# Kernel optimization log

Measured on AMD Instinct MI355X. Metric: run time of the kernel, lower is better.

## Reference

```python
import jax, jax.numpy as jnp
import numpy as np

DT = 0.001  # fixed dt in SimplifiedSSM.forward
LN_EPS = 1e-5


def _layernorm(x, g, b):
    m = jnp.mean(x, axis=-1, keepdims=True)
    v = jnp.mean(jnp.square(x - m), axis=-1, keepdims=True)
    return (x - m) * jax.lax.rsqrt(v + LN_EPS) * g + b


def setup_inputs() -> dict:
    key = jax.random.key(0)
    ks = jax.random.split(key, 12)
    Bn, C, H, W = 8, 1024, 32, 32
    depth, S = 4, 128
    d = C
    inp = {
        "x": jax.random.normal(ks[0], (Bn, C, H, W), dtype=jnp.float32),
        # SSM params, stacked over depth. A scaled by 0.1 for numerical stability
        # of the length-1024 recurrence (same math, tamer eigenvalues).
        "A": 0.1 * jax.random.normal(ks[1], (depth, S, S), dtype=jnp.float32),
        "Bp": jax.random.normal(ks[2], (depth, S, d), dtype=jnp.float32),
        "Cp": jax.random.normal(ks[3], (depth, d, S), dtype=jnp.float32),
        "Dp": jax.random.normal(ks[4], (depth, d), dtype=jnp.float32),
        # Linear layers (PyTorch convention: y = x @ W.T + b)
        "Wi": jax.random.normal(ks[5], (depth, d, d), dtype=jnp.float32) / np.sqrt(d),
        "bi": jax.random.normal(ks[6], (depth, d), dtype=jnp.float32) * 0.01,
        "Wo": jax.random.normal(ks[7], (depth, d, d), dtype=jnp.float32) / np.sqrt(d),
        "bo": jax.random.normal(ks[8], (depth, d), dtype=jnp.float32) * 0.01,
        # LayerNorm affine params
        "gamma": jnp.ones((depth, d), dtype=jnp.float32),
        "beta": jnp.zeros((depth, d), dtype=jnp.float32),
    }
    return inp


def reference(x, A, Bp, Cp, Dp, Wi, bi, Wo, bo, gamma, beta):
    Bn, C, H, W = x.shape
    depth, S, _ = A.shape
    # b c h w -> b (h w) c
    seq = x.reshape(Bn, C, H * W).transpose(0, 2, 1)
    eye = jnp.eye(S, dtype=x.dtype)
    for i in range(depth):
        n = _layernorm(seq, gamma[i], beta[i])
        u = n @ Wi[i].T + bi[i]                       # (B, L, d)
        A_bar = eye + DT * A[i]                       # (S, S)
        ub = jnp.einsum('bld,sd->lbs', u, DT * Bp[i]) # (L, B, S)

        def step(h, ub_t):
            h = h @ A_bar.T + ub_t
            return h, h

        h0 = jnp.zeros((Bn, S), dtype=x.dtype)
        _, hs = jax.lax.scan(step, h0, ub)            # hs: (L, B, S)
        y = jnp.einsum('lbs,ds->bld', hs, Cp[i]) + u * Dp[i]
        seq = seq + y @ Wo[i].T + bo[i]
    return seq.transpose(0, 2, 1).reshape(Bn, C, H, W)
```

## Files before the change

kernel.cpp:

```cpp
#include <hip/hip_runtime.h>
#include <stdint.h>

#define DT_STEP 0.001f
#define LN_EPS  1e-5f
#define Bn      8
#define Lseq    1024
#define Dm      1024
#define Sn      128
#define DEPTH   4
#define Mrows   (Bn * Lseq)
#define Qc      32
#define NCHUNK  (Lseq / Qc)
#define NPOW    33

typedef short bf16x8 __attribute__((ext_vector_type(8)));
typedef float f32x4  __attribute__((ext_vector_type(4)));

__device__ __forceinline__ unsigned short f2bf(float f) {
    unsigned int u = __float_as_uint(f);
    u += 0x7fffu + ((u >> 16) & 1u);
    return (unsigned short)(u >> 16);
}

#define GLOAD_LDS16(gp, lp)                                                \
    __builtin_amdgcn_global_load_lds(                                      \
        (const __attribute__((address_space(1))) unsigned int*)(gp),       \
        (__attribute__((address_space(3))) unsigned int*)(lp), 16, 0, 0)

__global__ __launch_bounds__(256) void prep_conv(const float* __restrict__ Wo,
                                                 const float* __restrict__ Dp,
                                                 const float* __restrict__ Bp,
                                                 unsigned short* __restrict__ Woh,
                                                 unsigned short* __restrict__ Wo2h,
                                                 unsigned short* __restrict__ Bph) {
    int z = blockIdx.y;
    int bx = blockIdx.x;
    if (bx < 1024) {
        int i = (bx * 256 + threadIdx.x) * 4;
        const float* S = Wo + (size_t)z * Dm * Dm;
        float4 v = *(const float4*)(S + i);
        int c = i & (Dm - 1);
        float4 d = *(const float4*)(Dp + (size_t)z * Dm + c);
        ushort4 o1, o2;
        o1.x = f2bf(v.x); o1.y = f2bf(v.y); o1.z = f2bf(v.z); o1.w = f2bf(v.w);
        o2.x = f2bf(v.x * d.x); o2.y = f2bf(v.y * d.y);
        o2.z = f2bf(v.z * d.z); o2.w = f2bf(v.w * d.w);
        *(ushort4*)(Woh  + (size_t)z * Dm * Dm + i) = o1;
        *(ushort4*)(Wo2h + (size_t)z * Dm * Dm + i) = o2;
    } else {
        int i = ((bx - 1024) * 256 + threadIdx.x) * 4;
        float4 v = *(const float4*)(Bp + (size_t)z * Sn * Dm + i);
        ushort4 o;
        o.x = f2bf(v.x); o.y = f2bf(v.y); o.z = f2bf(v.z); o.w = f2bf(v.w);
        *(ushort4*)(Bph + (size_t)z * Sn * Dm + i) = o;
    }
}

__global__ __launch_bounds__(256) void transpose_f2bf(const float* __restrict__ src,
                                                      unsigned short* __restrict__ dst,
                                                      int R, int C) {
    __shared__ float t[32][33];
    int z = blockIdx.z;
    const float* S = src + (size_t)z * R * C;
    unsigned short* D = dst + (size_t)z * R * C;
    int r0 = blockIdx.y * 32, c0 = blockIdx.x * 32;
    int tx = threadIdx.x & 31, ty = threadIdx.x >> 5;
    for (int rr = ty; rr < 32; rr += 8)
        t[rr][tx] = S[(size_t)(r0 + rr) * C + c0 + tx];
    __syncthreads();
    for (int rr = ty; rr < 32; rr += 8)
        D[(size_t)(c0 + rr) * R + r0 + tx] = f2bf(t[tx][rr]);
}

__global__ __launch_bounds__(256) void c2dt_boeff(const float* __restrict__ Bp,
                                                  const float* __restrict__ bi,
                                                  const float* __restrict__ Wo,
                                                  const float* __restrict__ Dp,
                                                  const float* __restrict__ bo,
                                                  float* __restrict__ c2dt,
                                                  float* __restrict__ boeff) {
    int z = blockIdx.x, j = blockIdx.y;
    int tid = threadIdx.x;
    float acc;
    if (j < Sn) {
        const float* br = Bp + ((size_t)z * Sn + j) * Dm;
        const float* bb = bi + (size_t)z * Dm;
        float4 v = *(const float4*)(br + tid * 4);
        float4 w = *(const float4*)(bb + tid * 4);
        acc = v.x * w.x + v.y * w.y + v.z * w.z + v.w * w.w;
    } else {
        int c = j - Sn;
        const float* wr = Wo + ((size_t)z * Dm + c) * Dm;
        const float* dp = Dp + (size_t)z * Dm;
        const float* bb = bi + (size_t)z * Dm;
        float4 w = *(const float4*)(wr + tid * 4);
        float4 d = *(const float4*)(dp + tid * 4);
        float4 b = *(const float4*)(bb + tid * 4);
        acc = w.x * d.x * b.x + w.y * d.y * b.y + w.z * d.z * b.z + w.w * d.w * b.w;
    }
#pragma unroll
    for (int off = 32; off > 0; off >>= 1) acc += __shfl_down(acc, off, 64);
    __shared__ float red[4];
    if ((tid & 63) == 0) red[tid >> 6] = acc;
    __syncthreads();
    if (tid == 0) {
        float tot = red[0] + red[1] + red[2] + red[3];
        if (j < Sn) c2dt[z * Sn + j] = DT_STEP * tot;
        else        boeff[(size_t)z * Dm + (j - Sn)] = bo[(size_t)z * Dm + (j - Sn)] + tot;
    }
}

__global__ __launch_bounds__(1024) void transpose_bll(const float* __restrict__ src,
                                                      float* __restrict__ dst) {
    __shared__ float tile[32][33];
    int b  = blockIdx.z;
    int i0 = blockIdx.y * 32, j0 = blockIdx.x * 32;
    int tx = threadIdx.x, ty = threadIdx.y;
    const float* S = src + (size_t)b * Dm * Lseq;
    float*       D = dst + (size_t)b * Dm * Lseq;
    tile[ty][tx] = S[(size_t)(j0 + ty) * 1024 + i0 + tx];
    __syncthreads();
    D[(size_t)(i0 + ty) * 1024 + j0 + tx] = tile[tx][ty];
}

__global__ __launch_bounds__(512) void ln_ub(
    const float* __restrict__ seq,
    unsigned short* __restrict__ nbuf,
    const unsigned short* __restrict__ M2,
    float* __restrict__ ub,
    const float* __restrict__ gam,
    const float* __restrict__ bet,
    const float* __restrict__ c2dtL) {
    __shared__ __align__(16) unsigned short As[256 * 8];
    __shared__ __align__(16) unsigned short Bs[1024 * 8];
    __shared__ float mrow[32], rrow[32];
    int row0 = blockIdx.x * 32;
    int tid = threadIdx.x;

    {
        int r = tid >> 4, l = tid & 15;
        const float* xr = seq + (size_t)(row0 + r) * Dm + l * 4;
        float s = 0.f, ss = 0.f;
#pragma unroll
        for (int j = 0; j < 16; j++) {
            float4 v = *(const float4*)(xr + j * 64);
            s  += v.x + v.y + v.z + v.w;
            ss += v.x * v.x + v.y * v.y + v.z * v.z + v.w * v.w;
        }
        s += __shfl_xor(s, 1, 16);  ss += __shfl_xor(ss, 1, 16);
        s += __shfl_xor(s, 2, 16);  ss += __shfl_xor(ss, 2, 16);
        s += __shfl_xor(s, 4, 16);  ss += __shfl_xor(ss, 4, 16);
        s += __shfl_xor(s, 8, 16);  ss += __shfl_xor(ss, 8, 16);
        if (l == 0) {
            float mean = s / (float)Dm;
            float var  = ss / (float)Dm - mean * mean;
            mrow[r] = mean;
            rrow[r] = rsqrtf(var + LN_EPS);
        }
    }
    __syncthreads();
#pragma unroll
    for (int g = 0; g < 8; g++) {
        int gi = tid + g * 512;
        int rA = gi >> 7, gc = gi & 127;
        int col = gc * 8;
        const float* p = seq + (size_t)(row0 + rA) * Dm + col;
        float4 v0 = *(const float4*)(p);
        float4 v1 = *(const float4*)(p + 4);
        float m = mrow[rA], rs = rrow[rA];
        float4 g0 = *(const float4*)(gam + col);
        float4 g1 = *(const float4*)(gam + col + 4);
        float4 b0 = *(const float4*)(bet + col);
        float4 b1 = *(const float4*)(bet + col + 4);
        bf16x8 pk;
        pk[0] = (short)f2bf((v0.x - m) * rs * g0.x + b0.x);
        pk[1] = (short)f2bf((v0.y - m) * rs * g0.y + b0.y);
        pk[2] = (short)f2bf((v0.z - m) * rs * g0.z + b0.z);
        pk[3] = (short)f2bf((v0.w - m) * rs * g0.w + b0.w);
        pk[4] = (short)f2bf((v1.x - m) * rs * g1.x + b1.x);
        pk[5] = (short)f2bf((v1.y - m) * rs * g1.y + b1.y);
        pk[6] = (short)f2bf((v1.z - m) * rs * g1.z + b1.z);
        pk[7] = (short)f2bf((v1.w - m) * rs * g1.w + b1.w);
        *(bf16x8*)(nbuf + (size_t)(row0 + rA) * Dm + col) = pk;
    }
    __syncthreads();

    int wave = tid >> 6, lane = tid & 63;
    int wn = wave * 16;
    int lr = lane & 15, lq = lane >> 4;

    int rowA = tid >> 3;
    int kclA = (tid & 7) ^ ((tid >> 3) & 7);
    int rowS[2], kclS[2], slotOff[2];
#pragma unroll
    for (int q = 0; q < 2; q++) {
        int s = tid + q * 512;
        rowS[q] = s >> 3;
        kclS[q] = (s & 7) ^ ((s >> 3) & 7);
        slotOff[q] = s * 8;
    }
    int aoff[2][2], boff[2];
#pragma unroll
    for (int i = 0; i < 2; i++)
#pragma unroll
        for (int h = 0; h < 2; h++) {
            int ra = i * 16 + lr;
            aoff[i][h] = (ra * 8 + ((lq + 4 * h) ^ (ra & 7))) * 8;
        }
#pragma unroll
    for (int h = 0; h < 2; h++) {
        int rn = wn + lr;
        boff[h] = (rn * 8 + ((lq + 4 * h) ^ (rn & 7))) * 8;
    }

    f32x4 acc[2];
#pragma unroll
    for (int i = 0; i < 2; i++) acc[i] = (f32x4){0.f, 0.f, 0.f, 0.f};

    for (int k0 = 0; k0 < Dm; k0 += 64) {
        const unsigned short* Abr = nbuf + (size_t)row0 * Dm + k0;
        const unsigned short* Bbr = M2 + k0;
        __syncthreads();
        if (tid < 256)
            GLOAD_LDS16(Abr + (size_t)rowA * Dm + kclA * 8, &As[tid * 8]);
#pragma unroll
        for (int q = 0; q < 2; q++)
            GLOAD_LDS16(Bbr + (size_t)rowS[q] * Dm + kclS[q] * 8, &Bs[slotOff[q]]);
        __syncthreads();
#pragma unroll
        for (int h = 0; h < 2; h++) {
            bf16x8 af[2], bfr;
#pragma unroll
            for (int i = 0; i < 2; i++) af[i] = *(const bf16x8*)&As[aoff[i][h]];
            bfr = *(const bf16x8*)&Bs[boff[h]];
#pragma unroll
            for (int i = 0; i < 2; i++)
                acc[i] = __builtin_amdgcn_mfma_f32_16x16x32_bf16(af[i], bfr,
                                                                 acc[i], 0, 0, 0);
        }
    }
#pragma unroll
    for (int i = 0; i < 2; i++)
#pragma unroll
        for (int r = 0; r < 4; r++) {
            int row = row0 + i * 16 + lq * 4 + r;
            int col = wn + lr;
            ub[(size_t)row * Sn + col] = acc[i][r] + c2dtL[col];
        }
}

__device__ __forceinline__ void gemm64_body(
    int flat, unsigned short* As, unsigned short* Bs,
    const unsigned short* __restrict__ A, const unsigned short* __restrict__ B,
    float* __restrict__ C, const float* __restrict__ bias, int K) {
    int rb = flat & 63, cb = flat >> 6;
    int row0 = rb * 128, col0 = cb * 64;
    int tid  = threadIdx.x;
    int wave = tid >> 6, lane = tid & 63;
    int wm = (wave & 1) * 64, wn = (wave >> 1) * 16;
    int lr = lane & 15, lq = lane >> 4;

    int rowS[2], kclS[2], slotOff[2];
#pragma unroll
    for (int q = 0; q < 2; q++) {
        int s = tid + q * 512;
        rowS[q] = s >> 3;
        kclS[q] = (s & 7) ^ ((s >> 3) & 7);
        slotOff[q] = s * 8;
    }
    int rowB = tid >> 3;
    int kclB = (tid & 7) ^ ((tid >> 3) & 7);

    int aoff[4][2], boff[2];
#pragma unroll
    for (int i = 0; i < 4; i++)
#pragma unroll
        for (int h = 0; h < 2; h++) {
            int ra = wm + i * 16 + lr;
            aoff[i][h] = (ra * 8 + ((lq + 4 * h) ^ (ra & 7))) * 8;
        }
#pragma unroll
    for (int h = 0; h < 2; h++) {
        int rn = wn + lr;
        boff[h] = (rn * 8 + ((lq + 4 * h) ^ (rn & 7))) * 8;
    }

    f32x4 acc[4];
#pragma unroll
    for (int i = 0; i < 4; i++) acc[i] = (f32x4){0.f, 0.f, 0.f, 0.f};

    for (int k0 = 0; k0 < K; k0 += 64) {
        const unsigned short* Abr = A + (size_t)row0 * K + k0;
        const unsigned short* Bbr = B + (size_t)col0 * K + k0;
        __syncthreads();
#pragma unroll
        for (int q = 0; q < 2; q++)
            GLOAD_LDS16(Abr + (size_t)rowS[q] * K + kclS[q] * 8, &As[slotOff[q]]);
        GLOAD_LDS16(Bbr + (size_t)rowB * K + kclB * 8, &Bs[tid * 8]);
        __syncthreads();
#pragma unroll
        for (int h = 0; h < 2; h++) {
            bf16x8 af[4], bf;
#pragma unroll
            for (int i = 0; i < 4; i++) af[i] = *(const bf16x8*)&As[aoff[i][h]];
            bf = *(const bf16x8*)&Bs[boff[h]];
#pragma unroll
            for (int i = 0; i < 4; i++)
                acc[i] = __builtin_amdgcn_mfma_f32_16x16x32_bf16(af[i], bf,
                                                                 acc[i], 0, 0, 0);
        }
    }
#pragma unroll
    for (int i = 0; i < 4; i++)
#pragma unroll
        for (int r = 0; r < 4; r++) {
            int row = row0 + wm + i * 16 + lq * 4 + r;
            int col = col0 + wn + lr;
            size_t idx = (size_t)row * Dm + col;
            float v = acc[i][r];
            if (bias) v += bias[col];
            C[idx] = C[idx] + v;
        }
}

__global__ __launch_bounds__(512) void gemm_w3k(const unsigned short* __restrict__ hs_bf,
                                                const unsigned short* __restrict__ W3,
                                                float* __restrict__ seq) {
    __shared__ __align__(16) unsigned short As[1024 * 8];
    __shared__ __align__(16) unsigned short Bs[512 * 8];
    gemm64_body(blockIdx.x, As, Bs, hs_bf, W3, seq, nullptr, Sn);
}

__global__ __launch_bounds__(512) void mega2(
    int mode, int nserial, int gemmFlat0,
    const unsigned short* __restrict__ nbuf,
    const unsigned short* __restrict__ W4,
    float* __restrict__ seq,
    const float* __restrict__ boeff,
    const float* __restrict__ ub,
    float* __restrict__ hs,
    unsigned short* __restrict__ hs_bf,
    const float* __restrict__ PowL,
    float* __restrict__ carryb) {
    __shared__ __align__(16) char smem[33280];
    int tid = threadIdx.x;

    if ((int)blockIdx.x >= nserial) {
        unsigned short* As = (unsigned short*)smem;
        unsigned short* Bs = (unsigned short*)(smem + 16384);
        gemm64_body(gemmFlat0 + (int)blockIdx.x - nserial, As, Bs,
                    nbuf, W4, seq, boeff, Dm);
        return;
    }

    if (mode == 0) {
        float* hsh = (float*)smem;
        float* hp  = hsh + 128;
        int chunk = blockIdx.x;
        int b = chunk >> 5, c = chunk & 31;
        int s = tid & 127, kq = tid >> 7;
        const float* Abar = PowL + (size_t)Sn * Sn;
        float arow[32];
#pragma unroll
        for (int j = 0; j < 32; j += 4) {
            float4 v = *(const float4*)(Abar + (size_t)s * Sn + kq * 32 + j);
            arow[j] = v.x; arow[j + 1] = v.y; arow[j + 2] = v.z; arow[j + 3] = v.w;
        }
        if (tid < 128) hsh[tid] = 0.f;
        __syncthreads();
        size_t base = (size_t)(b * Lseq + c * Qc) * Sn + s;
        float ut = (kq == 0) ? ub[base] : 0.f;
        const float* hq = &hsh[kq * 32];
        for (int t = 0; t < Qc; t++) {
            float utn = (kq == 0 && t + 1 < Qc) ? ub[base + (size_t)(t + 1) * Sn] : 0.f;
            float a0 = 0.f, a1 = 0.f, a2 = 0.f, a3 = 0.f;
#pragma unroll
            for (int j = 0; j < 32; j += 16) {
                float4 h0 = *(const float4*)&hq[j];
                float4 h1 = *(const float4*)&hq[j + 4];
                float4 h2 = *(const float4*)&hq[j + 8];
                float4 h3 = *(const float4*)&hq[j + 12];
                a0 += arow[j + 0] * h0.x + arow[j + 1] * h0.y + arow[j + 2] * h0.z + arow[j + 3] * h0.w;
                a1 += arow[j + 4] * h1.x + arow[j + 5] * h1.y + arow[j + 6] * h1.z + arow[j + 7] * h1.w;
                a2 += arow[j + 8] * h2.x + arow[j + 9] * h2.y + arow[j + 10] * h2.z + arow[j + 11] * h2.w;
                a3 += arow[j + 12] * h3.x + arow[j + 13] * h3.y + arow[j + 14] * h3.z + arow[j + 15] * h3.w;
            }
            hp[kq * 128 + s] = (a0 + a1) + (a2 + a3);
            __syncthreads();
            if (kq == 0) {
                float hv = ut + (hp[s] + hp[128 + s]) + (hp[256 + s] + hp[384 + s]);
                hs[base + (size_t)t * Sn] = hv;
                hsh[s] = hv;
            }
            __syncthreads();
            ut = utn;
        }
    } else if (mode == 1) {
        float* csh = (float*)smem;
        float* cp  = csh + 128;
        int b = blockIdx.x;
        int s = tid & 127, kq = tid >> 7;
        const float* AQ = PowL + (size_t)Qc * Sn * Sn;
        float arow[32];
#pragma unroll
        for (int j = 0; j < 32; j += 4) {
            float4 v = *(const float4*)(AQ + (size_t)s * Sn + kq * 32 + j);
            arow[j] = v.x; arow[j + 1] = v.y; arow[j + 2] = v.z; arow[j + 3] = v.w;
        }
        if (tid < 128) csh[tid] = 0.f;
        __syncthreads();
        float len = (kq == 0) ? hs[(size_t)(b * Lseq + Qc - 1) * Sn + s] : 0.f;
        const float* cq = &csh[kq * 32];
        for (int c = 0; c < NCHUNK; c++) {
            float le_c = len;
            len = (kq == 0 && c + 1 < NCHUNK)
                    ? hs[(size_t)(b * Lseq + (c + 1) * Qc + Qc - 1) * Sn + s] : 0.f;
            if (kq == 0) carryb[((size_t)b * NCHUNK + c) * Sn + s] = csh[s];
            float a0 = 0.f, a1 = 0.f, a2 = 0.f, a3 = 0.f;
#pragma unroll
            for (int j = 0; j < 32; j += 16) {
                float4 h0 = *(const float4*)&cq[j];
                float4 h1 = *(const float4*)&cq[j + 4];
                float4 h2 = *(const float4*)&cq[j + 8];
                float4 h3 = *(const float4*)&cq[j + 12];
                a0 += arow[j + 0] * h0.x + arow[j + 1] * h0.y + arow[j + 2] * h0.z + arow[j + 3] * h0.w;
                a1 += arow[j + 4] * h1.x + arow[j + 5] * h1.y + arow[j + 6] * h1.z + arow[j + 7] * h1.w;
                a2 += arow[j + 8] * h2.x + arow[j + 9] * h2.y + arow[j + 10] * h2.z + arow[j + 11] * h2.w;
                a3 += arow[j + 12] * h3.x + arow[j + 13] * h3.y + arow[j + 14] * h3.z + arow[j + 15] * h3.w;
            }
            cp[kq * 128 + s] = (a0 + a1) + (a2 + a3);
            __syncthreads();
            if (kq == 0)
                csh[s] = le_c + (cp[s] + cp[128 + s]) + (cp[256 + s] + cp[384 + s]);
            __syncthreads();
        }
    } else {
        float* Pl = (float*)smem;
        float* cl = (float*)(smem + 16896);
        int ser = blockIdx.x;
        int t = ser & 31, c4 = ser >> 5;
        const float* P = PowL + (size_t)(t + 1) * (Sn * Sn);
#pragma unroll
        for (int cc = 0; cc < 4; cc++)
            for (int idx = tid; idx < Bn * Sn; idx += 512)
                cl[cc * 1024 + idx] =
                    carryb[((size_t)(idx >> 7) * NCHUNK + (c4 * 4 + cc)) * Sn + (idx & 127)];
        int s = tid & 127, bh = tid >> 7;
        float acc[4][2];
#pragma unroll
        for (int cc = 0; cc < 4; cc++) { acc[cc][0] = 0.f; acc[cc][1] = 0.f; }
        for (int kh = 0; kh < 4; kh++) {
            __syncthreads();
            for (int idx = tid; idx < Sn * 32; idx += 512) {
                int r = idx >> 5, kk = idx & 31;
                Pl[r * 33 + kk] = P[(size_t)r * Sn + kh * 32 + kk];
            }
            __syncthreads();
            for (int kk = 0; kk < 32; kk++) {
                float pw = Pl[s * 33 + kk];
                int kg = kh * 32 + kk;
#pragma unroll
                for (int cc = 0; cc < 4; cc++)
#pragma unroll
                    for (int j = 0; j < 2; j++)
                        acc[cc][j] += pw * cl[cc * 1024 + (bh * 2 + j) * Sn + kg];
            }
        }
#pragma unroll
        for (int cc = 0; cc < 4; cc++) {
            int c = c4 * 4 + cc;
#pragma unroll
            for (int j = 0; j < 2; j++) {
                int bb = bh * 2 + j;
                size_t rowi = (size_t)(bb * Lseq + c * Qc + t) * Sn + s;
                hs_bf[rowi] = f2bf(hs[rowi] + acc[cc][j]);
            }
        }
    }
}

__global__ __launch_bounds__(512) void gemm_bk64(
    const unsigned short* __restrict__ A1, int sA1,
    const unsigned short* __restrict__ B1, int sB1,
    unsigned short* __restrict__ Ch,
    int ny, int N, int K, float scale,
    long batchA, long batchB, long batchC) {
    __shared__ __align__(16) unsigned short As[1024 * 8];
    __shared__ __align__(16) unsigned short Bs[1024 * 8];
    int flat = blockIdx.x;
    int rb = flat % ny, cb = flat / ny;
    int row0 = rb * 128, col0 = cb * 128;
    int z = blockIdx.y;
    int tid  = threadIdx.x;
    int wave = tid >> 6, lane = tid & 63;
    int wm = (wave & 1) * 64, wn = (wave >> 1) * 32;
    int lr = lane & 15, lq = lane >> 4;

    int rowS[2], kclS[2], slotOff[2];
#pragma unroll
    for (int q = 0; q < 2; q++) {
        int s = tid + q * 512;
        rowS[q] = s >> 3;
        kclS[q] = (s & 7) ^ ((s >> 3) & 7);
        slotOff[q] = s * 8;
    }
    int aoff[4][2], boff[2][2];
#pragma unroll
    for (int i = 0; i < 4; i++)
#pragma unroll
        for (int h = 0; h < 2; h++) {
            int ra = wm + i * 16 + lr;
            aoff[i][h] = (ra * 8 + ((lq + 4 * h) ^ (ra & 7))) * 8;
        }
#pragma unroll
    for (int j = 0; j < 2; j++)
#pragma unroll
        for (int h = 0; h < 2; h++) {
            int rn = wn + j * 16 + lr;
            boff[j][h] = (rn * 8 + ((lq + 4 * h) ^ (rn & 7))) * 8;
        }

    const unsigned short* Ab = A1 + (size_t)z * batchA;
    const unsigned short* Bb = B1 + (size_t)z * batchB + (size_t)col0 * sB1;

    f32x4 acc[4][2];
#pragma unroll
    for (int i = 0; i < 4; i++)
#pragma unroll
        for (int j = 0; j < 2; j++) acc[i][j] = (f32x4){0.f, 0.f, 0.f, 0.f};

    for (int k0 = 0; k0 < K; k0 += 64) {
        const unsigned short* Abr = Ab + (size_t)row0 * sA1 + k0;
        const unsigned short* Bbr = Bb + k0;
        __syncthreads();
#pragma unroll
        for (int q = 0; q < 2; q++) {
            GLOAD_LDS16(Abr + (size_t)rowS[q] * sA1 + kclS[q] * 8, &As[slotOff[q]]);
            GLOAD_LDS16(Bbr + (size_t)rowS[q] * sB1 + kclS[q] * 8, &Bs[slotOff[q]]);
        }
        __syncthreads();
#pragma unroll
        for (int h = 0; h < 2; h++) {
            bf16x8 af[4], bfr[2];
#pragma unroll
            for (int i = 0; i < 4; i++) af[i]  = *(const bf16x8*)&As[aoff[i][h]];
#pragma unroll
            for (int j = 0; j < 2; j++) bfr[j] = *(const bf16x8*)&Bs[boff[j][h]];
#pragma unroll
            for (int i = 0; i < 4; i++)
#pragma unroll
                for (int j = 0; j < 2; j++)
                    acc[i][j] = __builtin_amdgcn_mfma_f32_16x16x32_bf16(af[i], bfr[j],
                                                                       acc[i][j], 0, 0, 0);
        }
    }
#pragma unroll
    for (int i = 0; i < 4; i++)
#pragma unroll
        for (int j = 0; j < 2; j++)
#pragma unroll
            for (int r = 0; r < 4; r++) {
                int row = row0 + wm + i * 16 + lq * 4 + r;
                int col = col0 + wn + j * 16 + lr;
                Ch[(size_t)z * batchC + (size_t)row * N + col] = f2bf(acc[i][j][r] * scale);
            }
}

__global__ __launch_bounds__(128) void pow_init(const float* __restrict__ Amat,
                                                float* __restrict__ Pow) {
    int i = blockIdx.x;
    int s = blockIdx.y;
    int k = threadIdx.x;
    float eye = (s == k) ? 1.f : 0.f;
    size_t base = (size_t)i * NPOW * (Sn * Sn);
    Pow[base + (size_t)s * Sn + k] = eye;
    Pow[base + (size_t)(Sn * Sn) + (size_t)s * Sn + k] =
        eye + DT_STEP * Amat[(size_t)i * Sn * Sn + (size_t)s * Sn + k];
}

__global__ __launch_bounds__(256) void pow_mul(float* __restrict__ Pow, int m, int kmax) {
    int job = blockIdx.z;
    int i  = job / kmax;
    int kk = job % kmax + 1;
    const float* Pa = Pow + ((size_t)i * NPOW + m) * (Sn * Sn);
    const float* Pb = Pow + ((size_t)i * NPOW + kk) * (Sn * Sn);
    float*       Pc = Pow + ((size_t)i * NPOW + m + kk) * (Sn * Sn);
    int r0 = blockIdx.y * 64, c0 = blockIdx.x * 32;
    __shared__ float Asl[64 * 129];
    __shared__ float Bsl[128 * 32];
    int tx = threadIdx.x, ty = threadIdx.y;
    int tid = ty * 16 + tx;
    for (int idx = tid; idx < 64 * 128; idx += 256) {
        int r = idx >> 7, cc = idx & 127;
        Asl[r * 129 + cc] = Pa[(size_t)(r0 + r) * 128 + cc];
    }
    for (int idx = tid; idx < 128 * 32; idx += 256) {
        int r = idx >> 5, cc = idx & 31;
        Bsl[r * 32 + cc] = Pb[(size_t)r * 128 + c0 + cc];
    }
    __syncthreads();
    float acc[4][2] = {{0.f,0.f},{0.f,0.f},{0.f,0.f},{0.f,0.f}};
    for (int k = 0; k < 128; k++) {
        float b0 = Bsl[k * 32 + tx * 2];
        float b1 = Bsl[k * 32 + tx * 2 + 1];
#pragma unroll
        for (int r = 0; r < 4; r++) {
            float a = Asl[(ty * 4 + r) * 129 + k];
            acc[r][0] += a * b0;
            acc[r][1] += a * b1;
        }
    }
#pragma unroll
    for (int r = 0; r < 4; r++) {
        Pc[(size_t)(r0 + ty * 4 + r) * 128 + c0 + tx * 2]     = acc[r][0];
        Pc[(size_t)(r0 + ty * 4 + r) * 128 + c0 + tx * 2 + 1] = acc[r][1];
    }
}

extern "C" void kernel_launch(void* const* d_in, const int* in_sizes, int n_in,
                              void* d_out, int out_size, void* d_ws, size_t ws_size,
                              hipStream_t stream) {
    const float* x     = (const float*)d_in[0];
    const float* Am    = (const float*)d_in[1];
    const float* Bp    = (const float*)d_in[2];
    const float* Cp    = (const float*)d_in[3];
    const float* Dp    = (const float*)d_in[4];
    const float* Wi    = (const float*)d_in[5];
    const float* bi    = (const float*)d_in[6];
    const float* Wo    = (const float*)d_in[7];
    const float* bo    = (const float*)d_in[8];
    const float* gamma = (const float*)d_in[9];
    const float* beta  = (const float*)d_in[10];
    float* out = (float*)d_out;
    (void)in_sizes; (void)n_in; (void)out_size; (void)ws_size;

    char* ws = (char*)d_ws;
    float*          seq   = (float*)(ws + (size_t)0);
    unsigned short* nbuf  = (unsigned short*)(ws + (size_t)33554432);
    unsigned short* WiTh  = (unsigned short*)(ws + (size_t)33554432);
    unsigned short* Woh   = (unsigned short*)(ws + (size_t)41943040);
    unsigned short* W4h   = (unsigned short*)(ws + (size_t)50331648);
    float*          boeff = (float*)(ws + (size_t)58720256);
    float*          ub    = (float*)(ws + (size_t)67108864);
    float*          hs    = (float*)(ws + (size_t)71303168);
    unsigned short* hs_bf = (unsigned short*)(ws + (size_t)75497472);
    float*          Pow   = (float*)(ws + (size_t)77594624);
    float*          carry = (float*)(ws + (size_t)86245376);
    unsigned short* Wo2h  = (unsigned short*)(ws + (size_t)94765056);
    unsigned short* Bph   = (unsigned short*)(ws + (size_t)103153664);
    unsigned short* CpTh  = (unsigned short*)(ws + (size_t)104202240);
    unsigned short* M2h   = (unsigned short*)(ws + (size_t)105250816);
    unsigned short* W3h   = (unsigned short*)(ws + (size_t)106299392);
    float*          c2dt  = (float*)(ws + (size_t)107347968);

    const long WW = (long)Dm * Dm;
    const long SW = (long)Sn * Dm;

    hipLaunchKernelGGL(prep_conv, dim3(1024 + 128, DEPTH), dim3(256), 0, stream,
                       Wo, Dp, Bp, Woh, Wo2h, Bph);
    hipLaunchKernelGGL(transpose_f2bf, dim3(32, 32, DEPTH), dim3(256), 0, stream,
                       Wi, WiTh, Dm, Dm);
    hipLaunchKernelGGL(transpose_f2bf, dim3(4, 32, DEPTH), dim3(256), 0, stream,
                       Cp, CpTh, Dm, Sn);
    hipLaunchKernelGGL(c2dt_boeff, dim3(DEPTH, Sn + Dm), dim3(256), 0, stream,
                       Bp, bi, Wo, Dp, bo, c2dt, boeff);

    hipLaunchKernelGGL(gemm_bk64, dim3(8, DEPTH), dim3(512), 0, stream,
                       Bph, Dm, WiTh, Dm, M2h, 1, Dm, Dm, DT_STEP, SW, WW, SW);
    hipLaunchKernelGGL(gemm_bk64, dim3(8, DEPTH), dim3(512), 0, stream,
                       Woh, Dm, CpTh, Dm, W3h, 8, Sn, Dm, 1.f, WW, SW, SW);
    hipLaunchKernelGGL(gemm_bk64, dim3(8 * 8, DEPTH), dim3(512), 0, stream,
                       Wo2h, Dm, WiTh, Dm, W4h, 8, Dm, Dm, 1.f, WW, WW, WW);

    hipLaunchKernelGGL(transpose_bll, dim3(32, 32, Bn), dim3(32, 32), 0, stream, x, seq);

    hipLaunchKernelGGL(pow_init, dim3(DEPTH, Sn), dim3(Sn), 0, stream, Am, Pow);
    for (int m = 1; m < Qc; m <<= 1) {
        hipLaunchKernelGGL(pow_mul, dim3(4, 2, DEPTH * m), dim3(16, 16), 0, stream,
                           Pow, m, m);
    }

    for (int i = 0; i < DEPTH; i++) {
        const unsigned short* M2_i = M2h + (size_t)i * SW;
        const unsigned short* W3_i = W3h + (size_t)i * SW;
        const unsigned short* W4_i = W4h + (size_t)i * WW;
        const float* PowL = Pow + (size_t)i * NPOW * (Sn * Sn);

        hipLaunchKernelGGL(ln_ub, dim3(256), dim3(512), 0, stream,
                           seq, nbuf, M2_i, ub, gamma + i * Dm, beta + i * Dm,
                           c2dt + i * Sn);
        hipLaunchKernelGGL(mega2, dim3(256 + 512), dim3(512), 0, stream,
                           0, 256, 0, nbuf, W4_i, seq, boeff + i * Dm,
                           ub, hs, hs_bf, PowL, carry);
        hipLaunchKernelGGL(mega2, dim3(8 + 256), dim3(512), 0, stream,
                           1, 8, 512, nbuf, W4_i, seq, boeff + i * Dm,
                           ub, hs, hs_bf, PowL, carry);
        hipLaunchKernelGGL(mega2, dim3(256 + 256), dim3(512), 0, stream,
                           2, 256, 768, nbuf, W4_i, seq, boeff + i * Dm,
                           ub, hs, hs_bf, PowL, carry);
        hipLaunchKernelGGL(gemm_w3k, dim3(1024), dim3(512), 0, stream,
                           hs_bf, W3_i, seq);
    }

    hipLaunchKernelGGL(transpose_bll, dim3(32, 32, Bn), dim3(32, 32), 0, stream, seq, out);
}
```

Before: 715.6 us.

## Interleave serial-scan and GEMM blocks in mega2; rebalance tiles; merge prep GEMMs

The mega2 launches now interleave serial recurrence blocks with GEMM tile blocks by block index, so scan blocks spread across CUs and are dispatched early instead of sitting at the front of the grid. The 1024 W4 GEMM tiles are redistributed across the three phases: 256 in mode 0 (was 512), 256 in mode 1, and 512 in mode 2 (was 256), better matching each phase's serial latency. The three weight-precompute GEMM launches are merged into a single gemm_pre kernel with block-range dispatch, cutting launch overhead. The risk is worse overlap if the new tile split fits the serial phase lengths poorly.

```diff
diff --git a/kernel.cpp b/kernel.cpp
--- a/kernel.cpp
+++ b/kernel.cpp
@@ -323,16 +323,8 @@
         }
 }
 
-__global__ __launch_bounds__(512) void gemm_w3k(const unsigned short* __restrict__ hs_bf,
-                                                const unsigned short* __restrict__ W3,
-                                                float* __restrict__ seq) {
-    __shared__ __align__(16) unsigned short As[1024 * 8];
-    __shared__ __align__(16) unsigned short Bs[512 * 8];
-    gemm64_body(blockIdx.x, As, Bs, hs_bf, W3, seq, nullptr, Sn);
-}
-
 __global__ __launch_bounds__(512) void mega2(
-    int mode, int nserial, int gemmFlat0,
+    int mode,
     const unsigned short* __restrict__ nbuf,
     const unsigned short* __restrict__ W4,
     float* __restrict__ seq,
@@ -344,20 +336,27 @@
     float* __restrict__ carryb) {
     __shared__ __align__(16) char smem[33280];
     int tid = threadIdx.x;
-
-    if ((int)blockIdx.x >= nserial) {
+    int bid = blockIdx.x;
+
+    bool isSerial;
+    int sid, gflat;
+    if (mode == 0)      { isSerial = (bid & 1) == 0; sid = bid >> 1; gflat = bid >> 1; }
+    else if (mode == 1) { int q = bid / 33, r = bid % 33;
+                          isSerial = (r == 0); sid = q; gflat = 256 + q * 32 + r - 1; }
+    else                { int q = bid / 3, r = bid % 3;
+                          isSerial = (r == 0); sid = q; gflat = 512 + q * 2 + (r - 1); }
+
+    if (!isSerial) {
         unsigned short* As = (unsigned short*)smem;
         unsigned short* Bs = (unsigned short*)(smem + 16384);
-        gemm64_body(gemmFlat0 + (int)blockIdx.x - nserial, As, Bs,
-                    nbuf, W4, seq, boeff, Dm);
+        gemm64_body(gflat, As, Bs, nbuf, W4, seq, boeff, Dm);
         return;
     }
 
     if (mode == 0) {
         float* hsh = (float*)smem;
         float* hp  = hsh + 128;
-        int chunk = blockIdx.x;
-        int b = chunk >> 5, c = chunk & 31;
+        int b = sid >> 5, c = sid & 31;
         int s = tid & 127, kq = tid >> 7;
         const float* Abar = PowL + (size_t)Sn * Sn;
         float arow[32];
@@ -398,7 +397,7 @@
     } else if (mode == 1) {
         float* csh = (float*)smem;
         float* cp  = csh + 128;
-        int b = blockIdx.x;
+        int b = sid;
         int s = tid & 127, kq = tid >> 7;
         const float* AQ = PowL + (size_t)Qc * Sn * Sn;
         float arow[32];
@@ -437,8 +436,7 @@
     } else {
         float* Pl = (float*)smem;
         float* cl = (float*)(smem + 16896);
-        int ser = blockIdx.x;
-        int t = ser & 31, c4 = ser >> 5;
+        int t = sid & 31, c4 = sid >> 5;
         const float* P = PowL + (size_t)(t + 1) * (Sn * Sn);
 #pragma unroll
         for (int cc = 0; cc < 4; cc++)
@@ -479,18 +477,22 @@
     }
 }
 
-__global__ __launch_bounds__(512) void gemm_bk64(
-    const unsigned short* __restrict__ A1, int sA1,
-    const unsigned short* __restrict__ B1, int sB1,
-    unsigned short* __restrict__ Ch,
-    int ny, int N, int K, float scale,
-    long batchA, long batchB, long batchC) {
+__global__ __launch_bounds__(512) void gemm_w3k(const unsigned short* __restrict__ hs_bf,
+                                                const unsigned short* __restrict__ W3,
+                                                float* __restrict__ seq) {
     __shared__ __align__(16) unsigned short As[1024 * 8];
-    __shared__ __align__(16) unsigned short Bs[1024 * 8];
-    int flat = blockIdx.x;
+    __shared__ __align__(16) unsigned short Bs[512 * 8];
+    gemm64_body(blockIdx.x, As, Bs, hs_bf, W3, seq, nullptr, Sn);
+}
+
+__device__ __forceinline__ void gemm128_body(
+    int flat, int ny,
+    const unsigned short* __restrict__ A, int sA,
+    const unsigned short* __restrict__ Bz, int sB,
+    unsigned short* __restrict__ C, int N, int K, float scale,
+    unsigned short* As, unsigned short* Bs) {
     int rb = flat % ny, cb = flat / ny;
     int row0 = rb * 128, col0 = cb * 128;
-    int z = blockIdx.y;
     int tid  = threadIdx.x;
     int wave = tid >> 6, lane = tid & 63;
     int wm = (wave & 1) * 64, wn = (wave >> 1) * 32;
@@ -520,8 +522,7 @@
             boff[j][h] = (rn * 8 + ((lq + 4 * h) ^ (rn & 7))) * 8;
         }
 
-    const unsigned short* Ab = A1 + (size_t)z * batchA;
-    const unsigned short* Bb = B1 + (size_t)z * batchB + (size_t)col0 * sB1;
+    const unsigned short* Bb = Bz + (size_t)col0 * sB;
 
     f32x4 acc[4][2];
 #pragma unroll
@@ -530,13 +531,13 @@
         for (int j = 0; j < 2; j++) acc[i][j] = (f32x4){0.f, 0.f, 0.f, 0.f};
 
     for (int k0 = 0; k0 < K; k0 += 64) {
-        const unsigned short* Abr = Ab + (size_t)row0 * sA1 + k0;
+        const unsigned short* Abr = A + (size_t)row0 * sA + k0;
         const unsigned short* Bbr = Bb + k0;
         __syncthreads();
 #pragma unroll
         for (int q = 0; q < 2; q++) {
-            GLOAD_LDS16(Abr + (size_t)rowS[q] * sA1 + kclS[q] * 8, &As[slotOff[q]]);
-            GLOAD_LDS16(Bbr + (size_t)rowS[q] * sB1 + kclS[q] * 8, &Bs[slotOff[q]]);
+            GLOAD_LDS16(Abr + (size_t)rowS[q] * sA + kclS[q] * 8, &As[slotOff[q]]);
+            GLOAD_LDS16(Bbr + (size_t)rowS[q] * sB + kclS[q] * 8, &Bs[slotOff[q]]);
         }
         __syncthreads();
 #pragma unroll
@@ -562,8 +563,39 @@
             for (int r = 0; r < 4; r++) {
                 int row = row0 + wm + i * 16 + lq * 4 + r;
                 int col = col0 + wn + j * 16 + lr;
-                Ch[(size_t)z * batchC + (size_t)row * N + col] = f2bf(acc[i][j][r] * scale);
+                C[(size_t)row * N + col] = f2bf(acc[i][j][r] * scale);
             }
+}
+
+__global__ __launch_bounds__(512) void gemm_pre(
+    const unsigned short* __restrict__ Bph,
+    const unsigned short* __restrict__ WiTh,
+    unsigned short* __restrict__ M2h,
+    const unsigned short* __restrict__ Woh,
+    const unsigned short* __restrict__ CpTh,
+    unsigned short* __restrict__ W3h,
+    const unsigned short* __restrict__ Wo2h,
+    unsigned short* __restrict__ W4h) {
+    __shared__ __align__(16) unsigned short As[1024 * 8];
+    __shared__ __align__(16) unsigned short Bs[1024 * 8];
+    const long WW = (long)Dm * Dm;
+    const long SW = (long)Sn * Dm;
+    int bid = blockIdx.x;
+    if (bid < 32) {
+        int z = bid >> 3, flat = bid & 7;
+        gemm128_body(flat, 1, Bph + (size_t)z * SW, Dm, WiTh + (size_t)z * WW, Dm,
+                     M2h + (size_t)z * SW, Dm, Dm, DT_STEP, As, Bs);
+    } else if (bid < 64) {
+        int b2 = bid - 32;
+        int z = b2 >> 3, flat = b2 & 7;
+        gemm128_body(flat, 8, Woh + (size_t)z * WW, Dm, CpTh + (size_t)z * SW, Dm,
+                     W3h + (size_t)z * SW, Sn, Dm, 1.f, As, Bs);
+    } else {
+        int b3 = bid - 64;
+        int z = b3 >> 6, flat = b3 & 63;
+        gemm128_body(flat, 8, Wo2h + (size_t)z * WW, Dm, WiTh + (size_t)z * WW, Dm,
+                     W4h + (size_t)z * WW, Dm, Dm, 1.f, As, Bs);
+    }
 }
 
 __global__ __launch_bounds__(128) void pow_init(const float* __restrict__ Amat,
@@ -653,7 +685,6 @@
     unsigned short* W3h   = (unsigned short*)(ws + (size_t)106299392);
     float*          c2dt  = (float*)(ws + (size_t)107347968);
 
-    const long WW = (long)Dm * Dm;
     const long SW = (long)Sn * Dm;
 
     hipLaunchKernelGGL(prep_conv, dim3(1024 + 128, DEPTH), dim3(256), 0, stream,
@@ -665,12 +696,8 @@
     hipLaunchKernelGGL(c2dt_boeff, dim3(DEPTH, Sn + Dm), dim3(256), 0, stream,
                        Bp, bi, Wo, Dp, bo, c2dt, boeff);
 
-    hipLaunchKernelGGL(gemm_bk64, dim3(8, DEPTH), dim3(512), 0, stream,
-                       Bph, Dm, WiTh, Dm, M2h, 1, Dm, Dm, DT_STEP, SW, WW, SW);
-    hipLaunchKernelGGL(gemm_bk64, dim3(8, DEPTH), dim3(512), 0, stream,
-                       Woh, Dm, CpTh, Dm, W3h, 8, Sn, Dm, 1.f, WW, SW, SW);
-    hipLaunchKernelGGL(gemm_bk64, dim3(8 * 8, DEPTH), dim3(512), 0, stream,
-                       Wo2h, Dm, WiTh, Dm, W4h, 8, Dm, Dm, 1.f, WW, WW, WW);
+    hipLaunchKernelGGL(gemm_pre, dim3(320), dim3(512), 0, stream,
+                       Bph, WiTh, M2h, Woh, CpTh, W3h, Wo2h, W4h);
 
     hipLaunchKernelGGL(transpose_bll, dim3(32, 32, Bn), dim3(32, 32), 0, stream, x, seq);
 
@@ -683,20 +710,20 @@
     for (int i = 0; i < DEPTH; i++) {
         const unsigned short* M2_i = M2h + (size_t)i * SW;
         const unsigned short* W3_i = W3h + (size_t)i * SW;
-        const unsigned short* W4_i = W4h + (size_t)i * WW;
+        const unsigned short* W4_i = W4h + (size_t)i * (size_t)(Dm * Dm);
         const float* PowL = Pow + (size_t)i * NPOW * (Sn * Sn);
 
         hipLaunchKernelGGL(ln_ub, dim3(256), dim3(512), 0, stream,
                            seq, nbuf, M2_i, ub, gamma + i * Dm, beta + i * Dm,
                            c2dt + i * Sn);
-        hipLaunchKernelGGL(mega2, dim3(256 + 512), dim3(512), 0, stream,
-                           0, 256, 0, nbuf, W4_i, seq, boeff + i * Dm,
+        hipLaunchKernelGGL(mega2, dim3(512), dim3(512), 0, stream,
+                           0, nbuf, W4_i, seq, boeff + i * Dm,
                            ub, hs, hs_bf, PowL, carry);
-        hipLaunchKernelGGL(mega2, dim3(8 + 256), dim3(512), 0, stream,
-                           1, 8, 512, nbuf, W4_i, seq, boeff + i * Dm,
+        hipLaunchKernelGGL(mega2, dim3(264), dim3(512), 0, stream,
+                           1, nbuf, W4_i, seq, boeff + i * Dm,
                            ub, hs, hs_bf, PowL, carry);
-        hipLaunchKernelGGL(mega2, dim3(256 + 256), dim3(512), 0, stream,
-                           2, 256, 768, nbuf, W4_i, seq, boeff + i * Dm,
+        hipLaunchKernelGGL(mega2, dim3(768), dim3(512), 0, stream,
+                           2, nbuf, W4_i, seq, boeff + i * Dm,
                            ub, hs, hs_bf, PowL, carry);
         hipLaunchKernelGGL(gemm_w3k, dim3(1024), dim3(512), 0, stream,
                            hs_bf, W3_i, seq);
```

Result: no change. 705.4 us (-1.4%).
